# Kernel tuning notes

Measured on AMD Instinct MI355X. Metric: run time of the kernel, lower is better.

The kernel has to match this reference:

```python
import jax, jax.numpy as jnp
import numpy as np

B, T, HID, H = 2, 2048, 2048, 8
DK, DV = 256, 512          # head_qk_dim, head_v_dim
CHUNK = 64                 # chunk size used by fused_chunk retention
EPS = 1e-5


def setup_inputs() -> dict:
    key = jax.random.key(0)
    ks = jax.random.split(key, 7)
    s = 0.02  # ~ xavier_uniform with gain 2**-2.5
    return {
        "hidden_states": jax.random.normal(ks[0], (B, T, HID), jnp.float32),
        "Wq": jax.random.normal(ks[1], (HID, H * DK), jnp.float32) * s,
        "Wk": jax.random.normal(ks[2], (HID, H * DK), jnp.float32) * s,
        "Wv": jax.random.normal(ks[3], (HID, H * DV), jnp.float32) * s,
        "Wg": jax.random.normal(ks[4], (HID, H * DV), jnp.float32) * s,
        "Wo": jax.random.normal(ks[5], (H * DV, HID), jnp.float32) * s,
        "g_norm_w": jnp.ones((DV,), jnp.float32),
    }


def _rotary(x):
    # x: [B, T, H, D], non-interleaved rotary over full head dim, base 10000
    d = x.shape[-1]
    inv = 1.0 / (10000.0 ** (jnp.arange(0, d, 2, dtype=jnp.float32) / d))
    fr = jnp.arange(x.shape[1], dtype=jnp.float32)[:, None] * inv  # [T, d/2]
    cos = jnp.cos(fr)[None, :, None, :]
    sin = jnp.sin(fr)[None, :, None, :]
    x1, x2 = jnp.split(x, 2, axis=-1)
    return jnp.concatenate([x1 * cos - x2 * sin, x2 * cos + x1 * sin], axis=-1)


def _retention(q, k, v):
    # q,k: [B,H,T,DK]; v: [B,H,T,DV]; per-head decay gamma_h = 1 - 2^(-5-h)
    gamma = 1.0 - jnp.exp2(-5.0 - jnp.arange(H, dtype=jnp.float32))  # [H]
    q = q * (DK ** -0.5)
    N = T // CHUNK
    qc = q.reshape(B, H, N, CHUNK, DK).transpose(2, 0, 1, 3, 4)  # [N,B,H,C,K]
    kc = k.reshape(B, H, N, CHUNK, DK).transpose(2, 0, 1, 3, 4)
    vc = v.reshape(B, H, N, CHUNK, DV).transpose(2, 0, 1, 3, 4)
    i = jnp.arange(CHUNK, dtype=jnp.float32)
    # intra-chunk causal decay matrix D[h,i,j] = gamma_h^(i-j) for i>=j else 0
    Dm = jnp.where(i[:, None] >= i[None, :],
                   gamma[:, None, None] ** (i[:, None] - i[None, :]), 0.0)  # [H,C,C]
    qd = gamma[:, None] ** (i + 1.0)            # [H,C]: decay applied to q vs carried state
    kd = gamma[:, None] ** (CHUNK - 1.0 - i)    # [H,C]: decay applied to k for state update
    gC = gamma ** CHUNK                          # [H]

    def step(S, qkv):
        qcu, kcu, vcu = qkv  # [B,H,C,K], [B,H,C,K], [B,H,C,V]
        A = jnp.einsum('bhik,bhjk->bhij', qcu, kcu) * Dm[None]
        o_intra = jnp.einsum('bhij,bhjv->bhiv', A, vcu)
        o_inter = jnp.einsum('bhck,bhkv->bhcv', qcu * qd[None, :, :, None], S)
        kv = jnp.einsum('bhck,bhcv->bhkv', kcu * kd[None, :, :, None], vcu)
        S_new = gC[None, :, None, None] * S + kv
        return S_new, o_intra + o_inter

    S0 = jnp.zeros((B, H, DK, DV), jnp.float32)
    _, o = jax.lax.scan(step, S0, (qc, kc, vc))  # o: [N,B,H,C,V]
    return o.transpose(1, 2, 0, 3, 4).reshape(B, H, T, DV)


def reference(hidden_states, Wq, Wk, Wv, Wg, Wo, g_norm_w):
    q = (hidden_states @ Wq).reshape(B, T, H, DK)
    k = (hidden_states @ Wk).reshape(B, T, H, DK)
    v = (hidden_states @ Wv).reshape(B, T, H, DV)
    q = _rotary(q)
    k = _rotary(k)
    o = _retention(q.transpose(0, 2, 1, 3), k.transpose(0, 2, 1, 3),
                   v.transpose(0, 2, 1, 3))          # [B,H,T,DV]
    o = o.transpose(0, 2, 1, 3)                       # [B,T,H,DV]
    g = (hidden_states @ Wg).reshape(B, T, H, DV)
    # fused RMSNorm (per head_v_dim) + swish gate
    o = o * jax.lax.rsqrt(jnp.mean(o * o, axis=-1, keepdims=True) + EPS) * g_norm_w
    o = o * (g * jax.nn.sigmoid(g))
    return o.reshape(B, T, H * DV) @ Wo
```

## Files before the change

kernel.cpp:

```cpp
#include <hip/hip_runtime.h>
#include <cstdint>
#include <cstddef>

typedef __bf16 bf16;
typedef __bf16 bf16x8 __attribute__((ext_vector_type(8)));
typedef float  f32x4  __attribute__((ext_vector_type(4)));

#define MFMA16(a, b, c) __builtin_amdgcn_mfma_f32_16x16x32_bf16((a), (b), (c), 0, 0, 0)

__device__ __forceinline__ void async16(const bf16* g, bf16* l) {
  __builtin_amdgcn_global_load_lds(
      (const __attribute__((address_space(1))) unsigned int*)g,
      (__attribute__((address_space(3))) unsigned int*)l, 16, 0, 0);
}

__global__ __launch_bounds__(256) void k_cast(const float* __restrict__ x, bf16* __restrict__ y) {
  size_t i = ((size_t)blockIdx.x * 256 + threadIdx.x) * 4;
  float4 a = *(const float4*)(x + i);
  union { bf16 h[4]; uint2 u; } pk;
  pk.h[0] = (bf16)a.x; pk.h[1] = (bf16)a.y; pk.h[2] = (bf16)a.z; pk.h[3] = (bf16)a.w;
  *(uint2*)(y + i) = pk.u;
}

__global__ __launch_bounds__(256) void k_wt_all(const float* __restrict__ Wq,
                                                const float* __restrict__ Wk,
                                                const float* __restrict__ Wv,
                                                const float* __restrict__ Wg,
                                                bf16* __restrict__ WT) {
  const int K = 2048;
  __shared__ float tile[32][33];
  int z = blockIdx.z;
  const float* W; bf16* dst; int N;
  if (z == 0)      { W = Wq; dst = WT;                          N = 2048; }
  else if (z == 1) { W = Wk; dst = WT + (size_t)2048 * 2048;    N = 2048; }
  else if (z == 2) { W = Wv; dst = WT + (size_t)4096 * 2048;    N = 4096; }
  else             { W = Wg; dst = WT + (size_t)8192 * 2048;    N = 4096; }
  int n0 = blockIdx.x << 5;
  if (n0 >= N) return;
  int k0 = blockIdx.y << 5;
  int r = threadIdx.x >> 5, c = threadIdx.x & 31;
#pragma unroll
  for (int p = 0; p < 4; p++)
    tile[r + p * 8][c] = W[(size_t)(k0 + r + p * 8) * N + n0 + c];
  __syncthreads();
#pragma unroll
  for (int p = 0; p < 4; p++) {
    int nn = r + p * 8;
    dst[(size_t)(n0 + nn) * K + k0 + c] = (bf16)tile[c][nn];
  }
}

__global__ __launch_bounds__(256) void k_transpose_cast(const float* __restrict__ W,
                                                        bf16* __restrict__ WT, int K, int N) {
  __shared__ float tile[32][33];
  int k0 = blockIdx.y << 5, n0 = blockIdx.x << 5;
  int r = threadIdx.x >> 5, c = threadIdx.x & 31;
#pragma unroll
  for (int p = 0; p < 4; p++)
    tile[r + p * 8][c] = W[(size_t)(k0 + r + p * 8) * N + n0 + c];
  __syncthreads();
#pragma unroll
  for (int p = 0; p < 4; p++) {
    int nn = r + p * 8;
    WT[(size_t)(n0 + nn) * K + k0 + c] = (bf16)tile[c][nn];
  }
}

__global__ __launch_bounds__(256) void k_transpose_bh(const bf16* __restrict__ src,
                                                      bf16* __restrict__ dst, int D) {
  __shared__ bf16 tile[32][33];
  int bh = blockIdx.z;
  int b = bh >> 3, h = bh & 7;
  int d0 = blockIdx.x << 5, t0 = blockIdx.y << 5;
  int r = threadIdx.x >> 5, c = threadIdx.x & 31;
#pragma unroll
  for (int p = 0; p < 4; p++)
    tile[r + p * 8][c] = src[((size_t)((b * 2048 + t0 + r + p * 8) * 8 + h)) * D + d0 + c];
  __syncthreads();
#pragma unroll
  for (int p = 0; p < 4; p++)
    dst[((size_t)(bh * D + d0 + r + p * 8)) * 2048 + t0 + c] = tile[c][r + p * 8];
}

__global__ __launch_bounds__(256) void k_gemm_qkvg(const bf16* __restrict__ A,
                                                   const bf16* __restrict__ Bt,
                                                   bf16* __restrict__ qb, bf16* __restrict__ kb,
                                                   bf16* __restrict__ vbuf, bf16* __restrict__ gb) {
  const int K = 2048;
  __shared__ bf16 a_lds[128 * 64];
  __shared__ bf16 b_lds[128 * 64];
  int tid = threadIdx.x;
  int wave = tid >> 6, lane = tid & 63, quad = lane >> 4, l16 = lane & 15;
  int wr = wave >> 1, wc = wave & 1;
  int m0 = blockIdx.y << 7, n0 = blockIdx.x << 7;
  f32x4 acc[4][4] = {};
  int rl = tid >> 3;
  int sb = (tid & 7) ^ (rl & 7);
  const bf16* ag = A + (size_t)(m0 + rl) * K + sb * 8;
  const bf16* bg = Bt + (size_t)(n0 + rl) * K + sb * 8;
  bf16* al = a_lds + wave * 512;
  bf16* bl = b_lds + wave * 512;
  int sw = (l16 & 7) << 3;
  for (int kt = 0; kt < K; kt += 64) {
#pragma unroll
    for (int i = 0; i < 4; i++) {
      async16(ag + (size_t)i * 32 * K, al + i * 2048);
      async16(bg + (size_t)i * 32 * K, bl + i * 2048);
    }
    ag += 64; bg += 64;
    __syncthreads();
#pragma unroll
    for (int kk = 0; kk < 2; kk++) {
      int bo = ((kk * 4 + quad) << 3) ^ sw;
      bf16x8 af[4], bfv[4];
#pragma unroll
      for (int mt = 0; mt < 4; mt++)
        af[mt] = *(const bf16x8*)&a_lds[(wr * 64 + mt * 16 + l16) * 64 + bo];
#pragma unroll
      for (int nt = 0; nt < 4; nt++)
        bfv[nt] = *(const bf16x8*)&b_lds[(wc * 64 + nt * 16 + l16) * 64 + bo];
#pragma unroll
      for (int mt = 0; mt < 4; mt++)
#pragma unroll
        for (int nt = 0; nt < 4; nt++)
          acc[mt][nt] = MFMA16(af[mt], bfv[nt], acc[mt][nt]);
    }
    __syncthreads();
  }
  bf16* dst; int ldd, c0;
  if (n0 < 2048)       { dst = qb;   ldd = 2048; c0 = n0; }
  else if (n0 < 4096)  { dst = kb;   ldd = 2048; c0 = n0 - 2048; }
  else if (n0 < 8192)  { dst = vbuf; ldd = 4096; c0 = n0 - 4096; }
  else                 { dst = gb;   ldd = 4096; c0 = n0 - 8192; }
#pragma unroll
  for (int mt = 0; mt < 4; mt++)
#pragma unroll
    for (int nt = 0; nt < 4; nt++)
#pragma unroll
      for (int r = 0; r < 4; r++) {
        int row = m0 + wr * 64 + mt * 16 + quad * 4 + r;
        int col = c0 + wc * 64 + nt * 16 + l16;
        dst[(size_t)row * ldd + col] = (bf16)acc[mt][nt][r];
      }
}

__global__ __launch_bounds__(256) void k_gemm_bt(const bf16* __restrict__ A,
                                                 const bf16* __restrict__ Bt,
                                                 float* __restrict__ C, int M, int N, int K) {
  __shared__ bf16 a_lds[128 * 64];
  __shared__ bf16 b_lds[128 * 64];
  int tid = threadIdx.x;
  int wave = tid >> 6, lane = tid & 63, quad = lane >> 4, l16 = lane & 15;
  int wr = wave >> 1, wc = wave & 1;
  int m0 = blockIdx.y << 7, n0 = blockIdx.x << 7;
  f32x4 acc[4][4] = {};
  int rl = tid >> 3;
  int sb = (tid & 7) ^ (rl & 7);
  const bf16* ag = A + (size_t)(m0 + rl) * K + sb * 8;
  const bf16* bg = Bt + (size_t)(n0 + rl) * K + sb * 8;
  bf16* al = a_lds + wave * 512;
  bf16* bl = b_lds + wave * 512;
  int sw = (l16 & 7) << 3;
  for (int kt = 0; kt < K; kt += 64) {
#pragma unroll
    for (int i = 0; i < 4; i++) {
      async16(ag + (size_t)i * 32 * K, al + i * 2048);
      async16(bg + (size_t)i * 32 * K, bl + i * 2048);
    }
    ag += 64; bg += 64;
    __syncthreads();
#pragma unroll
    for (int kk = 0; kk < 2; kk++) {
      int bo = ((kk * 4 + quad) << 3) ^ sw;
      bf16x8 af[4], bfv[4];
#pragma unroll
      for (int mt = 0; mt < 4; mt++)
        af[mt] = *(const bf16x8*)&a_lds[(wr * 64 + mt * 16 + l16) * 64 + bo];
#pragma unroll
      for (int nt = 0; nt < 4; nt++)
        bfv[nt] = *(const bf16x8*)&b_lds[(wc * 64 + nt * 16 + l16) * 64 + bo];
#pragma unroll
      for (int mt = 0; mt < 4; mt++)
#pragma unroll
        for (int nt = 0; nt < 4; nt++)
          acc[mt][nt] = MFMA16(af[mt], bfv[nt], acc[mt][nt]);
    }
    __syncthreads();
  }
#pragma unroll
  for (int mt = 0; mt < 4; mt++)
#pragma unroll
    for (int nt = 0; nt < 4; nt++)
#pragma unroll
      for (int r = 0; r < 4; r++) {
        int row = m0 + wr * 64 + mt * 16 + quad * 4 + r;
        int col = n0 + wc * 64 + nt * 16 + l16;
        C[(size_t)row * N + col] = acc[mt][nt][r];
      }
}

__global__ __launch_bounds__(256) void k_rotary2(bf16* __restrict__ q, bf16* __restrict__ k) {
  int bid = blockIdx.x;
  bf16* x; int kmode;
  if (bid < 16384) { x = q; kmode = 0; }
  else             { x = k; kmode = 1; bid -= 16384; }
  int tid = threadIdx.x;
  int row = bid * 2 + (tid >> 7);
  int j = tid & 127;
  int t = (row >> 3) & 2047;
  int h = row & 7;
  float scale;
  if (kmode) {
    float lg = log2f(1.f - exp2f(-5.f - (float)h));
    scale = exp2f(lg * (float)(63 - (t & 63)));
  } else {
    scale = 0.0625f;
  }
  float inv = exp2f(-0.10381025296522976f * (float)j);
  float ang = (float)t * inv;
  float s, c;
  sincosf(ang, &s, &c);
  size_t base = (size_t)row * 256;
  float x1 = (float)x[base + j], x2 = (float)x[base + j + 128];
  x[base + j]       = (bf16)((x1 * c - x2 * s) * scale);
  x[base + j + 128] = (bf16)((x2 * c + x1 * s) * scale);
}

__global__ __launch_bounds__(256) void k_retention(const bf16* __restrict__ q,
                                                   const bf16* __restrict__ k,
                                                   const bf16* __restrict__ kT,
                                                   const bf16* __restrict__ vT,
                                                   bf16* __restrict__ o0,
                                                   bf16* __restrict__ o1) {
  __shared__ bf16 qA[2][64 * 128];
  __shared__ bf16 kA[2][64 * 128];
  __shared__ bf16 ktA[2][128 * 64];
  __shared__ bf16 vtA[2][64 * 64];
  __shared__ bf16 StA[2][64 * 136];

  int gid = blockIdx.x;
  int kh = gid & 1, h = (gid >> 1) & 7, b = (gid >> 4) & 1, vb = gid >> 5;
  bf16* oout = kh ? o1 : o0;
  int tid = threadIdx.x, lane = tid & 63, wave = tid >> 6, quad = lane >> 4, l16 = lane & 15;
  float gamma = 1.f - exp2f(-5.f - (float)h);
  float lg = log2f(gamma);
  float gC = exp2f(64.f * lg);
  int iRow = wave * 16 + l16;
  float ei = exp2f(lg * (float)(iRow - 63));
  float qd[4];
#pragma unroll
  for (int r = 0; r < 4; r++) qd[r] = exp2f(lg * (float)(wave * 16 + quad * 4 + r + 1));
  int sw = (l16 & 7) << 3;

  f32x4 S[2][4];
#pragma unroll
  for (int a = 0; a < 2; a++)
#pragma unroll
    for (int bb = 0; bb < 4; bb++) S[a][bb] = (f32x4){0.f, 0.f, 0.f, 0.f};

  auto stage = [&](int t0, int p) {
#pragma unroll 1
    for (int s = wave; s < 56; s += 4) {
      if (s < 16) {
        int i = s, c = i * 4 + (lane >> 4);
        int blk = (lane & 15) ^ (c & 7);
        async16(q + (((size_t)((b * 2048 + t0 + c) * 8 + h)) << 8) + kh * 128 + blk * 8,
                &qA[p][i * 512]);
      } else if (s < 32) {
        int i = s - 16, c = i * 4 + (lane >> 4);
        int blk = (lane & 15) ^ (c & 7);
        async16(k + (((size_t)((b * 2048 + t0 + c) * 8 + h)) << 8) + kh * 128 + blk * 8,
                &kA[p][i * 512]);
      } else if (s < 48) {
        int i = s - 32, kd = i * 8 + (lane >> 3);
        int blk = (lane & 7) ^ (kd & 7);
        async16(kT + ((size_t)((b * 8 + h) * 256 + kh * 128 + kd)) * 2048 + t0 + blk * 8,
                &ktA[p][i * 512]);
      } else {
        int i = s - 48, vd = i * 8 + (lane >> 3);
        int blk = (lane & 7) ^ (vd & 7);
        async16(vT + ((size_t)((b * 8 + h) * 512 + vb * 64 + vd)) * 2048 + t0 + blk * 8,
                &vtA[p][i * 512]);
      }
    }
  };

  stage(0, 0);

  for (int n = 0; n < 32; n++) {
    int p = n & 1, t0 = n * 64;
#pragma unroll
    for (int a = 0; a < 2; a++)
#pragma unroll
      for (int bb = 0; bb < 4; bb++) {
        int k0 = wave * 32 + a * 16 + quad * 4;
        int vc = bb * 16 + l16;
        f32x4 s = S[a][bb];
        union { bf16 hh[4]; unsigned long long u; } pkk;
        pkk.hh[0] = (bf16)s[0]; pkk.hh[1] = (bf16)s[1];
        pkk.hh[2] = (bf16)s[2]; pkk.hh[3] = (bf16)s[3];
        *(unsigned long long*)&StA[p][vc * 136 + k0] = pkk.u;
      }
    __syncthreads();
    if (n < 31) stage(t0 + 64, 1 - p);

    bf16x8 qf[4];
#pragma unroll
    for (int kk = 0; kk < 4; kk++)
      qf[kk] = *(const bf16x8*)&qA[p][iRow * 128 + ((((kk * 4 + quad) << 3)) ^ sw)];

    f32x4 Dt[4];
#pragma unroll
    for (int jt = 0; jt < 4; jt++) {
      Dt[jt] = (f32x4){0.f, 0.f, 0.f, 0.f};
#pragma unroll
      for (int kk = 0; kk < 4; kk++) {
        bf16x8 kf = *(const bf16x8*)&kA[p][(jt * 16 + l16) * 128 + ((((kk * 4 + quad) << 3)) ^ sw)];
        Dt[jt] = MFMA16(kf, qf[kk], Dt[jt]);
      }
    }
    unsigned pkA[4][2];
#pragma unroll
    for (int jt = 0; jt < 4; jt++) {
      int j0 = jt * 16 + quad * 4;
      union { bf16 hh[2]; unsigned u; } p0, p1;
      p0.hh[0] = (bf16)((iRow >= j0 + 0) ? Dt[jt][0] * ei : 0.f);
      p0.hh[1] = (bf16)((iRow >= j0 + 1) ? Dt[jt][1] * ei : 0.f);
      p1.hh[0] = (bf16)((iRow >= j0 + 2) ? Dt[jt][2] * ei : 0.f);
      p1.hh[1] = (bf16)((iRow >= j0 + 3) ? Dt[jt][3] * ei : 0.f);
      pkA[jt][0] = p0.u; pkA[jt][1] = p1.u;
    }
    int s0b = ((((quad & 1) << 5) + l16) << 2);
    int s1b = s0b + 64;
    bool hi = (quad >> 1) != 0;
    bf16x8 afA[2];
#pragma unroll
    for (int kk = 0; kk < 2; kk++) {
      unsigned x00 = __builtin_amdgcn_ds_bpermute(s0b, (int)pkA[2 * kk][0]);
      unsigned x01 = __builtin_amdgcn_ds_bpermute(s0b, (int)pkA[2 * kk][1]);
      unsigned x10 = __builtin_amdgcn_ds_bpermute(s0b, (int)pkA[2 * kk + 1][0]);
      unsigned x11 = __builtin_amdgcn_ds_bpermute(s0b, (int)pkA[2 * kk + 1][1]);
      unsigned y00 = __builtin_amdgcn_ds_bpermute(s1b, (int)pkA[2 * kk][0]);
      unsigned y01 = __builtin_amdgcn_ds_bpermute(s1b, (int)pkA[2 * kk][1]);
      unsigned y10 = __builtin_amdgcn_ds_bpermute(s1b, (int)pkA[2 * kk + 1][0]);
      unsigned y11 = __builtin_amdgcn_ds_bpermute(s1b, (int)pkA[2 * kk + 1][1]);
      union { unsigned u[4]; bf16x8 v; } rr;
      rr.u[0] = hi ? x10 : x00;
      rr.u[1] = hi ? x11 : x01;
      rr.u[2] = hi ? y10 : y00;
      rr.u[3] = hi ? y11 : y01;
      afA[kk] = rr.v;
    }

    f32x4 oacc[4];
#pragma unroll
    for (int nt = 0; nt < 4; nt++) {
      oacc[nt] = (f32x4){0.f, 0.f, 0.f, 0.f};
#pragma unroll
      for (int kk = 0; kk < 4; kk++) {
        bf16x8 stf = *(const bf16x8*)&StA[p][(nt * 16 + l16) * 136 + kk * 32 + quad * 8];
        oacc[nt] = MFMA16(qf[kk], stf, oacc[nt]);
      }
    }
#pragma unroll
    for (int nt = 0; nt < 4; nt++)
#pragma unroll
      for (int r = 0; r < 4; r++) oacc[nt][r] *= qd[r];

    bf16x8 vtf[4][2];
#pragma unroll
    for (int nt = 0; nt < 4; nt++)
#pragma unroll
      for (int kk = 0; kk < 2; kk++)
        vtf[nt][kk] = *(const bf16x8*)&vtA[p][(nt * 16 + l16) * 64 + ((((kk * 4 + quad) << 3)) ^ sw)];
#pragma unroll
    for (int nt = 0; nt < 4; nt++)
#pragma unroll
      for (int kk = 0; kk < 2; kk++)
        oacc[nt] = MFMA16(afA[kk], vtf[nt][kk], oacc[nt]);

#pragma unroll
    for (int nt = 0; nt < 4; nt++)
#pragma unroll
      for (int r = 0; r < 4; r++) {
        int row = t0 + wave * 16 + quad * 4 + r;
        int col = vb * 64 + nt * 16 + l16;
        oout[((size_t)((b * 2048 + row) * 8 + h)) * 512 + col] = (bf16)oacc[nt][r];
      }

#pragma unroll
    for (int a = 0; a < 2; a++) {
      bf16x8 ktf[2];
#pragma unroll
      for (int kk = 0; kk < 2; kk++)
        ktf[kk] = *(const bf16x8*)&ktA[p][(wave * 32 + a * 16 + l16) * 64 + ((((kk * 4 + quad) << 3)) ^ sw)];
#pragma unroll
      for (int bb = 0; bb < 4; bb++) {
        f32x4 cc = S[a][bb] * gC;
#pragma unroll
        for (int kk = 0; kk < 2; kk++) cc = MFMA16(ktf[kk], vtf[bb][kk], cc);
        S[a][bb] = cc;
      }
    }
  }
}

__global__ __launch_bounds__(256) void k_normgate(const bf16* __restrict__ o0,
                                                  const bf16* __restrict__ o1,
                                                  const bf16* __restrict__ g,
                                                  const float* __restrict__ gw,
                                                  bf16* __restrict__ og) {
  int tid = threadIdx.x, lane = tid & 63;
  size_t row = (size_t)blockIdx.x * 4 + (tid >> 6);
  size_t base = row * 512;
  float vv[8];
  float ss = 0.f;
#pragma unroll
  for (int hh = 0; hh < 2; hh++) {
    int col = hh * 256 + lane * 4;
    union { bf16 h[4]; uint2 u; } a, b2;
    a.u = *(const uint2*)(o0 + base + col);
    b2.u = *(const uint2*)(o1 + base + col);
#pragma unroll
    for (int jj = 0; jj < 4; jj++) {
      float v = (float)a.h[jj] + (float)b2.h[jj];
      vv[hh * 4 + jj] = v;
      ss += v * v;
    }
  }
#pragma unroll
  for (int off = 1; off < 64; off <<= 1) ss += __shfl_xor(ss, off, 64);
  float rinv = rsqrtf(ss * (1.0f / 512.0f) + 1e-5f);
#pragma unroll
  for (int hh = 0; hh < 2; hh++) {
    int col = hh * 256 + lane * 4;
    union { bf16 h[4]; uint2 u; } gp;
    gp.u = *(const uint2*)(g + base + col);
    union { bf16 h[4]; uint2 u; } op;
#pragma unroll
    for (int jj = 0; jj < 4; jj++) {
      float gg = (float)gp.h[jj];
      float y = vv[hh * 4 + jj] * rinv * gw[col + jj] * (gg / (1.f + expf(-gg)));
      op.h[jj] = (bf16)y;
    }
    *(uint2*)(og + base + col) = op.u;
  }
}

extern "C" void kernel_launch(void* const* d_in, const int* in_sizes, int n_in,
                              void* d_out, int out_size, void* d_ws, size_t ws_size,
                              hipStream_t stream) {
  (void)in_sizes; (void)n_in; (void)out_size; (void)ws_size;
  const float* hs = (const float*)d_in[0];
  const float* Wq = (const float*)d_in[1];
  const float* Wk = (const float*)d_in[2];
  const float* Wv = (const float*)d_in[3];
  const float* Wg = (const float*)d_in[4];
  const float* Wo = (const float*)d_in[5];
  const float* gw = (const float*)d_in[6];
  float* out = (float*)d_out;

  char* ws = (char*)d_ws;
  const size_t MB = 1024 * 1024;
  bf16* hid = (bf16*)(ws + 0);
  bf16* WT  = (bf16*)(ws + 16 * MB);
  bf16* qb  = (bf16*)(ws + 64 * MB);
  bf16* kb  = (bf16*)(ws + 80 * MB);
  bf16* vbuf= (bf16*)(ws + 96 * MB);
  bf16* gb  = (bf16*)(ws + 128 * MB);
  bf16* kT  = (bf16*)(ws + 160 * MB);
  bf16* vT  = (bf16*)(ws + 176 * MB);
  bf16* o0  = (bf16*)(ws + 0);
  bf16* o1  = (bf16*)(ws + 32 * MB);
  bf16* og  = (bf16*)(ws + 160 * MB);
  bf16* WoT = (bf16*)(ws + 192 * MB);

  k_cast<<<8192, 256, 0, stream>>>(hs, hid);
  k_wt_all<<<dim3(128, 64, 4), 256, 0, stream>>>(Wq, Wk, Wv, Wg, WT);

  k_gemm_qkvg<<<dim3(96, 32), 256, 0, stream>>>(hid, WT, qb, kb, vbuf, gb);

  k_rotary2<<<32768, 256, 0, stream>>>(qb, kb);

  k_transpose_bh<<<dim3(8, 64, 16), 256, 0, stream>>>(kb, kT, 256);
  k_transpose_bh<<<dim3(16, 64, 16), 256, 0, stream>>>(vbuf, vT, 512);

  k_retention<<<256, 256, 0, stream>>>(qb, kb, kT, vT, o0, o1);

  k_transpose_cast<<<dim3(64, 128), 256, 0, stream>>>(Wo, WoT, 4096, 2048);
  k_normgate<<<8192, 256, 0, stream>>>(o0, o1, gb, gw, og);
  k_gemm_bt<<<dim3(16, 32), 256, 0, stream>>>(og, WoT, out, 4096, 2048, 4096);
}
```

Measured before the change: 669.3 us.

## Split retention over narrower value blocks and read q/k fragments from global memory

The retention kernel now tiles the value dimension in 32-column blocks instead of 64, which doubles the grid from 256 to 512 workgroups so more CUs have work. To cut shared memory per block, the q and k chunk tiles are no longer staged in LDS but read directly from global memory into MFMA fragments. The state buffer is single-buffered, with an extra barrier per chunk. In exchange, q, k and the intra-chunk QK^T product are recomputed by twice as many blocks, and the direct global loads may add latency.

```diff
diff --git a/kernel.cpp b/kernel.cpp
--- a/kernel.cpp
+++ b/kernel.cpp
@@ -232,14 +232,13 @@
                                                    const bf16* __restrict__ vT,
                                                    bf16* __restrict__ o0,
                                                    bf16* __restrict__ o1) {
-  __shared__ bf16 qA[2][64 * 128];
-  __shared__ bf16 kA[2][64 * 128];
   __shared__ bf16 ktA[2][128 * 64];
-  __shared__ bf16 vtA[2][64 * 64];
-  __shared__ bf16 StA[2][64 * 136];
+  __shared__ bf16 vtA[2][32 * 64];
+  __shared__ bf16 StA[32 * 136];
 
   int gid = blockIdx.x;
   int kh = gid & 1, h = (gid >> 1) & 7, b = (gid >> 4) & 1, vb = gid >> 5;
+  int bh = b * 8 + h;
   bf16* oout = kh ? o1 : o0;
   int tid = threadIdx.x, lane = tid & 63, wave = tid >> 6, quad = lane >> 4, l16 = lane & 15;
   float gamma = 1.f - exp2f(-5.f - (float)h);
@@ -252,34 +251,27 @@
   for (int r = 0; r < 4; r++) qd[r] = exp2f(lg * (float)(wave * 16 + quad * 4 + r + 1));
   int sw = (l16 & 7) << 3;
 
-  f32x4 S[2][4];
+  const bf16* qrow = q + ((size_t)(b * 2048) * 8 + h) * 256 + kh * 128;
+  const bf16* krow = k + ((size_t)(b * 2048) * 8 + h) * 256 + kh * 128;
+
+  f32x4 S[2][2];
 #pragma unroll
   for (int a = 0; a < 2; a++)
 #pragma unroll
-    for (int bb = 0; bb < 4; bb++) S[a][bb] = (f32x4){0.f, 0.f, 0.f, 0.f};
+    for (int bb = 0; bb < 2; bb++) S[a][bb] = (f32x4){0.f, 0.f, 0.f, 0.f};
 
   auto stage = [&](int t0, int p) {
 #pragma unroll 1
-    for (int s = wave; s < 56; s += 4) {
+    for (int s = wave; s < 20; s += 4) {
       if (s < 16) {
-        int i = s, c = i * 4 + (lane >> 4);
-        int blk = (lane & 15) ^ (c & 7);
-        async16(q + (((size_t)((b * 2048 + t0 + c) * 8 + h)) << 8) + kh * 128 + blk * 8,
-                &qA[p][i * 512]);
-      } else if (s < 32) {
-        int i = s - 16, c = i * 4 + (lane >> 4);
-        int blk = (lane & 15) ^ (c & 7);
-        async16(k + (((size_t)((b * 2048 + t0 + c) * 8 + h)) << 8) + kh * 128 + blk * 8,
-                &kA[p][i * 512]);
-      } else if (s < 48) {
-        int i = s - 32, kd = i * 8 + (lane >> 3);
+        int kd = s * 8 + (lane >> 3);
         int blk = (lane & 7) ^ (kd & 7);
-        async16(kT + ((size_t)((b * 8 + h) * 256 + kh * 128 + kd)) * 2048 + t0 + blk * 8,
-                &ktA[p][i * 512]);
+        async16(kT + ((size_t)(bh * 256 + kh * 128 + kd)) * 2048 + t0 + blk * 8,
+                &ktA[p][s * 512]);
       } else {
-        int i = s - 48, vd = i * 8 + (lane >> 3);
+        int i = s - 16, vd = i * 8 + (lane >> 3);
         int blk = (lane & 7) ^ (vd & 7);
-        async16(vT + ((size_t)((b * 8 + h) * 512 + vb * 64 + vd)) * 2048 + t0 + blk * 8,
+        async16(vT + ((size_t)(bh * 512 + vb * 32 + vd)) * 2048 + t0 + blk * 8,
                 &vtA[p][i * 512]);
       }
     }
@@ -292,14 +284,14 @@
 #pragma unroll
     for (int a = 0; a < 2; a++)
 #pragma unroll
-      for (int bb = 0; bb < 4; bb++) {
+      for (int bb = 0; bb < 2; bb++) {
         int k0 = wave * 32 + a * 16 + quad * 4;
         int vc = bb * 16 + l16;
         f32x4 s = S[a][bb];
         union { bf16 hh[4]; unsigned long long u; } pkk;
         pkk.hh[0] = (bf16)s[0]; pkk.hh[1] = (bf16)s[1];
         pkk.hh[2] = (bf16)s[2]; pkk.hh[3] = (bf16)s[3];
-        *(unsigned long long*)&StA[p][vc * 136 + k0] = pkk.u;
+        *(unsigned long long*)&StA[vc * 136 + k0] = pkk.u;
       }
     __syncthreads();
     if (n < 31) stage(t0 + 64, 1 - p);
@@ -307,7 +299,7 @@
     bf16x8 qf[4];
 #pragma unroll
     for (int kk = 0; kk < 4; kk++)
-      qf[kk] = *(const bf16x8*)&qA[p][iRow * 128 + ((((kk * 4 + quad) << 3)) ^ sw)];
+      qf[kk] = *(const bf16x8*)(qrow + (size_t)(t0 + iRow) * 2048 + kk * 32 + quad * 8);
 
     f32x4 Dt[4];
 #pragma unroll
@@ -315,7 +307,7 @@
       Dt[jt] = (f32x4){0.f, 0.f, 0.f, 0.f};
 #pragma unroll
       for (int kk = 0; kk < 4; kk++) {
-        bf16x8 kf = *(const bf16x8*)&kA[p][(jt * 16 + l16) * 128 + ((((kk * 4 + quad) << 3)) ^ sw)];
+        bf16x8 kf = *(const bf16x8*)(krow + (size_t)(t0 + jt * 16 + l16) * 2048 + kk * 32 + quad * 8);
         Dt[jt] = MFMA16(kf, qf[kk], Dt[jt]);
       }
     }
@@ -352,39 +344,39 @@
       afA[kk] = rr.v;
     }
 
-    f32x4 oacc[4];
-#pragma unroll
-    for (int nt = 0; nt < 4; nt++) {
+    f32x4 oacc[2];
+#pragma unroll
+    for (int nt = 0; nt < 2; nt++) {
       oacc[nt] = (f32x4){0.f, 0.f, 0.f, 0.f};
 #pragma unroll
       for (int kk = 0; kk < 4; kk++) {
-        bf16x8 stf = *(const bf16x8*)&StA[p][(nt * 16 + l16) * 136 + kk * 32 + quad * 8];
+        bf16x8 stf = *(const bf16x8*)&StA[(nt * 16 + l16) * 136 + kk * 32 + quad * 8];
         oacc[nt] = MFMA16(qf[kk], stf, oacc[nt]);
       }
     }
 #pragma unroll
-    for (int nt = 0; nt < 4; nt++)
+    for (int nt = 0; nt < 2; nt++)
 #pragma unroll
       for (int r = 0; r < 4; r++) oacc[nt][r] *= qd[r];
 
-    bf16x8 vtf[4][2];
-#pragma unroll
-    for (int nt = 0; nt < 4; nt++)
+    bf16x8 vtf[2][2];
+#pragma unroll
+    for (int nt = 0; nt < 2; nt++)
 #pragma unroll
       for (int kk = 0; kk < 2; kk++)
         vtf[nt][kk] = *(const bf16x8*)&vtA[p][(nt * 16 + l16) * 64 + ((((kk * 4 + quad) << 3)) ^ sw)];
 #pragma unroll
-    for (int nt = 0; nt < 4; nt++)
+    for (int nt = 0; nt < 2; nt++)
 #pragma unroll
       for (int kk = 0; kk < 2; kk++)
         oacc[nt] = MFMA16(afA[kk], vtf[nt][kk], oacc[nt]);
 
 #pragma unroll
-    for (int nt = 0; nt < 4; nt++)
+    for (int nt = 0; nt < 2; nt++)
 #pragma unroll
       for (int r = 0; r < 4; r++) {
         int row = t0 + wave * 16 + quad * 4 + r;
-        int col = vb * 64 + nt * 16 + l16;
+        int col = vb * 32 + nt * 16 + l16;
         oout[((size_t)((b * 2048 + row) * 8 + h)) * 512 + col] = (bf16)oacc[nt][r];
       }
 
@@ -395,13 +387,14 @@
       for (int kk = 0; kk < 2; kk++)
         ktf[kk] = *(const bf16x8*)&ktA[p][(wave * 32 + a * 16 + l16) * 64 + ((((kk * 4 + quad) << 3)) ^ sw)];
 #pragma unroll
-      for (int bb = 0; bb < 4; bb++) {
+      for (int bb = 0; bb < 2; bb++) {
         f32x4 cc = S[a][bb] * gC;
 #pragma unroll
         for (int kk = 0; kk < 2; kk++) cc = MFMA16(ktf[kk], vtf[bb][kk], cc);
         S[a][bb] = cc;
       }
     }
+    __syncthreads();
   }
 }
 
@@ -485,7 +478,7 @@
   k_transpose_bh<<<dim3(8, 64, 16), 256, 0, stream>>>(kb, kT, 256);
   k_transpose_bh<<<dim3(16, 64, 16), 256, 0, stream>>>(vbuf, vT, 512);
 
-  k_retention<<<256, 256, 0, stream>>>(qb, kb, kT, vT, o0, o1);
+  k_retention<<<512, 256, 0, stream>>>(qb, kb, kT, vT, o0, o1);
 
   k_transpose_cast<<<dim3(64, 128), 256, 0, stream>>>(Wo, WoT, 4096, 2048);
   k_normgate<<<8192, 256, 0, stream>>>(o0, o1, gb, gw, og);
```

Result: slower. 717.3 us (+7.2%).
